# Performance work log

Measured on AMD Instinct MI355X. Metric: run time of the kernel, lower is better.

The kernel has to match this reference:

```python
import jax, jax.numpy as jnp
import numpy as np

N, E, X_DIM, EA_DIM, HID, NL, NC, NGRAPH = 50000, 800000, 64, 16, 64, 3, 10, 64
BN_EPS = 1e-5
STD_EPS = 1e-5


def setup_inputs() -> dict:
    key = jax.random.key(0)
    ks = jax.random.split(key, 24)
    w = lambda k, sh: (jax.random.normal(k, sh, jnp.float32) * 0.05)
    inp = {
        'x': jax.random.normal(ks[0], (N, X_DIM), jnp.float32),
        'edge_index': jax.random.randint(ks[1], (2, E), 0, N),
        'batch': jnp.sort(jax.random.randint(ks[2], (N,), 0, NGRAPH)),
        'edge_attr': jax.random.normal(ks[3], (E, EA_DIM), jnp.float32),
        # node / edge encoders
        'node_w': w(ks[4], (X_DIM, HID)), 'node_b': jnp.zeros((HID,), jnp.float32),
        'edge_w': w(ks[5], (EA_DIM, HID)), 'edge_b': jnp.zeros((HID,), jnp.float32),
        # per-layer PNA post_nn Linear(12*3*HID -> HID) and BatchNorm
        'conv_w': w(ks[6], (NL, 12 * 3 * HID, HID)), 'conv_b': jnp.zeros((NL, HID), jnp.float32),
        'bn_g': jnp.ones((NL, HID), jnp.float32), 'bn_b': jnp.zeros((NL, HID), jnp.float32),
        # fc_out: HID -> HID/2 -> HID/4 -> NC
        'fc1_w': w(ks[7], (HID, HID // 2)), 'fc1_b': jnp.zeros((HID // 2,), jnp.float32),
        'fc2_w': w(ks[8], (HID // 2, HID // 4)), 'fc2_b': jnp.zeros((HID // 4,), jnp.float32),
        'fc3_w': w(ks[9], (HID // 4, NC)), 'fc3_b': jnp.zeros((NC,), jnp.float32),
    }
    return inp


def _pna_layer(x, src, dst, ea, deg, degc, log_deg, avg_log, w, b):
    # message: concat([x_i, x_j, edge_attr]) with x_i = x[dst], x_j = x[src]  -> [E, 3H]
    h = jnp.concatenate([x[dst], x[src], ea], axis=-1)
    inv = (1.0 / degc)[:, None]
    s1 = jax.ops.segment_sum(h, dst, num_segments=N)
    mean = s1 * inv
    mean_sq = jax.ops.segment_sum(h * h, dst, num_segments=N) * inv
    std = jnp.sqrt(jax.nn.relu(mean_sq - mean * mean) + STD_EPS)
    has = (deg > 0)[:, None]
    mx = jax.ops.segment_max(h, dst, num_segments=N)
    mx = jnp.where(has, mx, 0.0)
    mn = -jax.ops.segment_max(-h, dst, num_segments=N)
    mn = jnp.where(has, mn, 0.0)
    out = jnp.concatenate([mean, mn, mx, std], axis=-1)  # [N, 4*3H]
    amp = (log_deg / avg_log)[:, None]
    att = (avg_log / log_deg)[:, None]
    out = jnp.concatenate([out, out * amp, out * att], axis=-1)  # [N, 12*3H]
    return out @ w + b


def reference(x, edge_index, batch, edge_attr, node_w, node_b, edge_w, edge_b,
              conv_w, conv_b, bn_g, bn_b, fc1_w, fc1_b, fc2_w, fc2_b, fc3_w, fc3_b):
    src, dst = edge_index[0], edge_index[1]
    x = x @ node_w + node_b
    ea = edge_attr @ edge_w + edge_b
    deg = jax.ops.segment_sum(jnp.ones((E,), jnp.float32), dst, num_segments=N)
    degc = jnp.maximum(deg, 1.0)
    log_deg = jnp.log(degc + 1.0)
    # avg of log(deg+1) over nodes (equivalent to the histogram-based avg_deg['log'])
    avg_log = jnp.mean(jnp.log(deg + 1.0))
    for i in range(NL):
        h = _pna_layer(x, src, dst, ea, deg, degc, log_deg, avg_log, conv_w[i], conv_b[i])
        mu = jnp.mean(h, axis=0)
        var = jnp.mean((h - mu) ** 2, axis=0)  # biased var, as torch BN training mode
        h = (h - mu) * jax.lax.rsqrt(var + BN_EPS) * bn_g[i] + bn_b[i]
        x = jax.nn.relu(h) + x  # dropout is identity in eval
    # global mean pool over graphs
    gsum = jax.ops.segment_sum(x, batch, num_segments=NGRAPH)
    gcnt = jnp.maximum(jax.ops.segment_sum(jnp.ones((N,), jnp.float32), batch, num_segments=NGRAPH), 1.0)
    g = gsum / gcnt[:, None]
    g = jax.nn.relu(g @ fc1_w + fc1_b)
    g = jax.nn.relu(g @ fc2_w + fc2_b)
    return g @ fc3_w + fc3_b
```

## Files before the change

kernel.cpp:

```cpp
#include <hip/hip_runtime.h>
#include <math.h>

#define N_NODES 50000
#define N_EDGES 800000
#define NGRAPH  64
#define KEFF    576

typedef short bf16x8 __attribute__((ext_vector_type(8)));
typedef float f32x4  __attribute__((ext_vector_type(4)));

__device__ inline unsigned short f2bf_rne(float f) {
  unsigned u = __float_as_uint(f);
  unsigned r = u + 0x7FFFu + ((u >> 16) & 1u);
  return (unsigned short)(r >> 16);
}
__device__ inline float bf2f(unsigned short h) {
  return __uint_as_float(((unsigned)h) << 16);
}


__global__ __launch_bounds__(256) void zero_kernel(
    int* __restrict__ cnt, float* __restrict__ gsum,
    double* __restrict__ bnacc, double* __restrict__ avgacc)
{
  int i = blockIdx.x * 256 + threadIdx.x;
  if (i < N_NODES) { cnt[i] = 0; return; }
  int j = i - N_NODES;
  if (j < NGRAPH * 64) { gsum[j] = 0.f; return; }
  int k = j - NGRAPH * 64;
  if (k < 3 * 128) { bnacc[k] = 0.0; return; }
  if (k == 3 * 128) *avgacc = 0.0;
}

__global__ __launch_bounds__(256) void node_enc_kernel(
    const float* __restrict__ xin, const float* __restrict__ nw,
    const float* __restrict__ nb, float* __restrict__ x)
{
  __shared__ float xs[256];
  int tid = threadIdx.x;
  int base = blockIdx.x * 256;
  xs[tid] = xin[base + tid];
  __syncthreads();
  int r = tid >> 6, j = tid & 63;
  float acc = nb[j];
#pragma unroll
  for (int t = 0; t < 64; t++) acc = fmaf(xs[r * 64 + t], nw[t * 64 + j], acc);
  x[base + tid] = acc;
}

__global__ void count_kernel(const int* __restrict__ dst, int* __restrict__ cnt)
{
  int e = blockIdx.x * 256 + threadIdx.x;
  atomicAdd(&cnt[dst[e]], 1);
}

__global__ __launch_bounds__(256) void scan_a_kernel(
    const int* __restrict__ cnt, int* __restrict__ bsum)
{
  __shared__ int s[256];
  int i = blockIdx.x * 256 + threadIdx.x;
  s[threadIdx.x] = (i < N_NODES) ? cnt[i] : 0;
  __syncthreads();
  for (int off = 128; off > 0; off >>= 1) {
    if (threadIdx.x < off) s[threadIdx.x] += s[threadIdx.x + off];
    __syncthreads();
  }
  if (threadIdx.x == 0) bsum[blockIdx.x] = s[0];
}

__global__ __launch_bounds__(256) void scan_b_kernel(
    const int* __restrict__ bsum, int* __restrict__ boff)
{
  __shared__ int s[256];
  int tid = threadIdx.x;
  int v = (tid < 196) ? bsum[tid] : 0;
  s[tid] = v;
  __syncthreads();
  for (int off = 1; off < 256; off <<= 1) {
    int t = (tid >= off) ? s[tid - off] : 0;
    __syncthreads();
    s[tid] += t;
    __syncthreads();
  }
  boff[tid] = s[tid] - v;
}

__global__ __launch_bounds__(256) void scan_c_kernel(
    const int* __restrict__ cnt, const int* __restrict__ boff,
    int* __restrict__ row_ptr, int* __restrict__ cursor)
{
  __shared__ int s[256];
  int tid = threadIdx.x;
  int i = blockIdx.x * 256 + tid;
  int v = (i < N_NODES) ? cnt[i] : 0;
  s[tid] = v;
  __syncthreads();
  for (int off = 1; off < 256; off <<= 1) {
    int t = (tid >= off) ? s[tid - off] : 0;
    __syncthreads();
    s[tid] += t;
    __syncthreads();
  }
  int incl = s[tid];
  int base = boff[blockIdx.x];
  if (i < N_NODES) { row_ptr[i] = base + incl - v; cursor[i] = base + incl - v; }
  if (i == N_NODES - 1) row_ptr[N_NODES] = base + incl;
}

__global__ void fill_kernel(const int* __restrict__ src, const int* __restrict__ dst,
                            int* __restrict__ cursor, int* __restrict__ srcs,
                            int* __restrict__ eids)
{
  int e = blockIdx.x * 256 + threadIdx.x;
  int d = dst[e];
  int pos = atomicAdd(&cursor[d], 1);
  srcs[pos] = src[e];
  eids[pos] = e;
}

__global__ __launch_bounds__(256) void deg_log_kernel(
    const int* __restrict__ cnt, float* __restrict__ log_deg,
    double* __restrict__ avgacc)
{
  __shared__ double sb[256];
  int i = blockIdx.x * 256 + threadIdx.x;
  double c = 0.0;
  if (i < N_NODES) {
    int d = cnt[i];
    int dc = d > 0 ? d : 1;
    log_deg[i] = logf((float)dc + 1.0f);
    c = (double)logf((float)d + 1.0f);
  }
  sb[threadIdx.x] = c;
  __syncthreads();
  for (int off = 128; off > 0; off >>= 1) {
    if (threadIdx.x < off) sb[threadIdx.x] += sb[threadIdx.x + off];
    __syncthreads();
  }
  if (threadIdx.x == 0) atomicAdd(avgacc, sb[0]);
}

__global__ void avg_gb_kernel(const double* __restrict__ avgacc,
                              float* __restrict__ avgf,
                              const int* __restrict__ batch,
                              int* __restrict__ gcnt)
{
  __shared__ int sb[65];
  int g = threadIdx.x;
  int lo = 0, hi = N_NODES;
  while (lo < hi) { int mid = (lo + hi) >> 1; if (batch[mid] < g) lo = mid + 1; else hi = mid; }
  sb[g] = lo;
  if (g == 0) { sb[64] = N_NODES; *avgf = (float)(*avgacc / (double)N_NODES); }
  __syncthreads();
  gcnt[g] = sb[g + 1] - sb[g];
}


__global__ __launch_bounds__(256) void wprep_kernel(
    const float* __restrict__ conv_w, unsigned short* __restrict__ wh,
    unsigned short* __restrict__ wl)
{
  int idx = blockIdx.x * 256 + threadIdx.x;
  int k = idx % 576;
  int c = (idx / 576) % 192;
  int l = idx / (576 * 192);
  int s = c >> 6, j = c & 63;
  const float* CW = conv_w + (size_t)l * 2304 * 64;
  float v;
  if (k < 64) {
    int base = s * 768 + k;
    v = CW[base * 64 + j] + CW[(base + 192) * 64 + j] + CW[(base + 384) * 64 + j];
  } else {
    const int srcseg[8] = {1, 2, 4, 5, 7, 8, 10, 11};
    int q = (k >> 6) - 1;
    int t = k & 63;
    v = CW[(s * 768 + srcseg[q] * 64 + t) * 64 + j];
  }
  unsigned short hh = f2bf_rne(v);
  size_t o = (((size_t)l * 12 + (c >> 4)) * 72 + (k >> 3)) * 128 + (c & 15) * 8 + (k & 7);
  wh[o] = hh;
  wl[o] = f2bf_rne(v - bf2f(hh));
}

__global__ void bprep_kernel(const float* __restrict__ conv_w, float* __restrict__ beff)
{
  int l = blockIdx.x;
  int s = threadIdx.x >> 6, j = threadIdx.x & 63;
  const float* CW = conv_w + (size_t)l * 2304 * 64 + (size_t)(s * 768 + 576) * 64;
  float sum = 0.f;
#pragma unroll
  for (int t = 0; t < 64; t++) sum += CW[t * 64 + j];
  beff[(l * 3 + s) * 64 + j] = sum * 0.0031622776601683794f;
}


__global__ __launch_bounds__(256) void agg_e_kernel(
    const float* __restrict__ eattr, const float* __restrict__ edge_w,
    const float* __restrict__ edge_b, const int* __restrict__ row_ptr,
    const int* __restrict__ eids,
    unsigned short* __restrict__ agg_h, unsigned short* __restrict__ agg_l)
{
  int lane = threadIdx.x & 63;
  int quad = lane >> 4, a16 = lane & 15;
  int n = blockIdx.x * 4 + (threadIdx.x >> 6);
  if (n >= N_NODES) return;
  float ew[16];
#pragma unroll
  for (int t = 0; t < 16; t++) ew[t] = edge_w[t * 64 + lane];
  float eb = edge_b[lane];
  int s0 = row_ptr[n], s1 = row_ptr[n + 1];
  float se = 0.f, qe = 0.f, mxe = -3.4e38f, mne = 3.4e38f;

  for (int j = s0; j < s1; j += 4) {
    int idx = j + quad;
    float av = 0.f;
    if (idx < s1) av = eattr[(size_t)eids[idx] * 16 + a16];
    unsigned au = __float_as_uint(av);
    float ea[4];
#pragma unroll
    for (int q = 0; q < 4; q++) {
      float c0 = eb, c1 = 0.f;
#pragma unroll
      for (int t = 0; t < 8; t++) {
        c0 = fmaf(__uint_as_float(__builtin_amdgcn_readlane(au, q * 16 + t)), ew[t], c0);
        c1 = fmaf(__uint_as_float(__builtin_amdgcn_readlane(au, q * 16 + 8 + t)), ew[8 + t], c1);
      }
      ea[q] = c0 + c1;
    }
    int rem = s1 - j;
#pragma unroll
    for (int q = 0; q < 4; q++) {
      if (q < rem) {
        se += ea[q]; qe = fmaf(ea[q], ea[q], qe);
        mxe = fmaxf(mxe, ea[q]); mne = fminf(mne, ea[q]);
      }
    }
  }

  int deg = s1 - s0;
  float inv = 1.0f / fmaxf((float)deg, 1.0f);
  bool has = deg > 0;
  float m_e = se * inv, ms_e = qe * inv;
  float sd_e = sqrtf(fmaxf(ms_e - m_e * m_e, 0.f) + 1e-5f);
  float mx_e = has ? mxe : 0.f, mn_e = has ? mne : 0.f;

  unsigned short* bh = agg_h + (size_t)n * KEFF;
  unsigned short* bl = agg_l + (size_t)n * KEFF;
#define W2(off, val) { float _v = (val); unsigned short _h = f2bf_rne(_v); \
                       bh[(off) + lane] = _h; bl[(off) + lane] = f2bf_rne(_v - bf2f(_h)); }
  W2(128, m_e); W2(256, mn_e); W2(384, mx_e); W2(512, sd_e);
#undef W2
}


__global__ __launch_bounds__(256) void agg_x_kernel(
    const float* __restrict__ x, const int* __restrict__ srcs,
    const int* __restrict__ row_ptr,
    unsigned short* __restrict__ agg_h, unsigned short* __restrict__ agg_l)
{
  int lane = threadIdx.x & 63;
  int n = blockIdx.x * 4 + (threadIdx.x >> 6);
  if (n >= N_NODES) return;
  float xd = x[(size_t)n * 64 + lane];
  int s0 = row_ptr[n], s1 = row_ptr[n + 1];
  float sA = 0.f, sB = 0.f, sC = 0.f, sD = 0.f;
  float qA = 0.f, qB = 0.f, qC = 0.f, qD = 0.f;
  float mx0 = -3.4e38f, mx1 = -3.4e38f, mn0 = 3.4e38f, mn1 = 3.4e38f;
  int j = s0;
  for (; j + 7 < s1; j += 8) {
    int e0 = srcs[j],     e1 = srcs[j + 1], e2 = srcs[j + 2], e3 = srcs[j + 3];
    int e4 = srcs[j + 4], e5 = srcs[j + 5], e6 = srcs[j + 6], e7 = srcs[j + 7];
    float x0 = x[(size_t)e0 * 64 + lane];
    float x1 = x[(size_t)e1 * 64 + lane];
    float x2 = x[(size_t)e2 * 64 + lane];
    float x3 = x[(size_t)e3 * 64 + lane];
    float x4 = x[(size_t)e4 * 64 + lane];
    float x5 = x[(size_t)e5 * 64 + lane];
    float x6 = x[(size_t)e6 * 64 + lane];
    float x7 = x[(size_t)e7 * 64 + lane];
    sA += x0; sB += x1; sC += x2; sD += x3;
    sA += x4; sB += x5; sC += x6; sD += x7;
    qA = fmaf(x0, x0, qA); qB = fmaf(x1, x1, qB);
    qC = fmaf(x2, x2, qC); qD = fmaf(x3, x3, qD);
    qA = fmaf(x4, x4, qA); qB = fmaf(x5, x5, qB);
    qC = fmaf(x6, x6, qC); qD = fmaf(x7, x7, qD);
    mx0 = fmaxf(mx0, fmaxf(fmaxf(x0, x1), fmaxf(x2, x3)));
    mx1 = fmaxf(mx1, fmaxf(fmaxf(x4, x5), fmaxf(x6, x7)));
    mn0 = fminf(mn0, fminf(fminf(x0, x1), fminf(x2, x3)));
    mn1 = fminf(mn1, fminf(fminf(x4, x5), fminf(x6, x7)));
  }
  if (j < s1) {
    int last = s1 - 1;
    int rem = s1 - j;
    int e0 = srcs[j];
    int e1 = srcs[j + 1 < s1 ? j + 1 : last];
    int e2 = srcs[j + 2 < s1 ? j + 2 : last];
    int e3 = srcs[j + 3 < s1 ? j + 3 : last];
    int e4 = srcs[j + 4 < s1 ? j + 4 : last];
    int e5 = srcs[j + 5 < s1 ? j + 5 : last];
    int e6 = srcs[j + 6 < s1 ? j + 6 : last];
    int e7 = srcs[j + 7 < s1 ? j + 7 : last];
    float x0 = x[(size_t)e0 * 64 + lane];
    float x1 = x[(size_t)e1 * 64 + lane];
    float x2 = x[(size_t)e2 * 64 + lane];
    float x3 = x[(size_t)e3 * 64 + lane];
    float x4 = x[(size_t)e4 * 64 + lane];
    float x5 = x[(size_t)e5 * 64 + lane];
    float x6 = x[(size_t)e6 * 64 + lane];
    float x7 = x[(size_t)e7 * 64 + lane];
    mx0 = fmaxf(mx0, fmaxf(fmaxf(x0, x1), fmaxf(x2, x3)));
    mx1 = fmaxf(mx1, fmaxf(fmaxf(x4, x5), fmaxf(x6, x7)));
    mn0 = fminf(mn0, fminf(fminf(x0, x1), fminf(x2, x3)));
    mn1 = fminf(mn1, fminf(fminf(x4, x5), fminf(x6, x7)));
    float z1 = 1 < rem ? x1 : 0.f;
    float z2 = 2 < rem ? x2 : 0.f;
    float z3 = 3 < rem ? x3 : 0.f;
    float z4 = 4 < rem ? x4 : 0.f;
    float z5 = 5 < rem ? x5 : 0.f;
    float z6 = 6 < rem ? x6 : 0.f;
    float z7 = 7 < rem ? x7 : 0.f;
    sA += x0; sB += z1; sC += z2; sD += z3;
    sA += z4; sB += z5; sC += z6; sD += z7;
    qA = fmaf(x0, x0, qA); qB = fmaf(z1, z1, qB);
    qC = fmaf(z2, z2, qC); qD = fmaf(z3, z3, qD);
    qA = fmaf(z4, z4, qA); qB = fmaf(z5, z5, qB);
    qC = fmaf(z6, z6, qC); qD = fmaf(z7, z7, qD);
  }
  float sx = (sA + sB) + (sC + sD);
  float qx = (qA + qB) + (qC + qD);
  float mxx = fmaxf(mx0, mx1), mnx = fminf(mn0, mn1);

  int deg = s1 - s0;
  float inv = 1.0f / fmaxf((float)deg, 1.0f);
  bool has = deg > 0;
  float m_s = sx * inv, ms_s = qx * inv;
  float sd_s = sqrtf(fmaxf(ms_s - m_s * m_s, 0.f) + 1e-5f);
  float mx_s = has ? mxx : 0.f, mn_s = has ? mnx : 0.f;

  unsigned short* bh = agg_h + (size_t)n * KEFF;
  unsigned short* bl = agg_l + (size_t)n * KEFF;
#define W2(off, val) { float _v = (val); unsigned short _h = f2bf_rne(_v); \
                       bh[(off) + lane] = _h; bl[(off) + lane] = f2bf_rne(_v - bf2f(_h)); }
  W2(0,   has ? xd : 0.f);
  W2(64,  m_s); W2(192, mn_s); W2(320, mx_s); W2(448, sd_s);
#undef W2
}


__global__ __launch_bounds__(256, 3) void gemm_kernel(
    const unsigned short* __restrict__ Ah, const unsigned short* __restrict__ Al,
    const unsigned short* __restrict__ Wh, const unsigned short* __restrict__ Wl,
    const float* __restrict__ beff, const float* __restrict__ bias,
    const float* __restrict__ log_deg, const float* __restrict__ avg_ptr,
    float* __restrict__ h, double* __restrict__ bnacc)
{
  __shared__ __align__(16) short AsH[64 * 40], AsL[64 * 40];
  int tid = threadIdx.x;
  int lane = tid & 63, w = tid >> 6;
  int quad = lane >> 4, l15 = lane & 15;
  int n0 = blockIdx.x * 64;

  int arow = tid >> 2, ac = tid & 3;
  int an = n0 + arow; if (an >= N_NODES) an = N_NODES - 1;
  const unsigned short* gah = Ah + (size_t)an * KEFF + ac * 8;
  const unsigned short* gal = Al + (size_t)an * KEFF + ac * 8;

  const unsigned short* pbh[3];
  const unsigned short* pbl[3];
#pragma unroll
  for (int s = 0; s < 3; s++) {
    size_t cb = (size_t)(s * 4 + w) * 72 * 128 + l15 * 8;
    pbh[s] = Wh + cb;
    pbl[s] = Wl + cb;
  }

  f32x4 acc[4][3] = {};
  float4 rh = *(const float4*)(gah);
  float4 rl = *(const float4*)(gal);

  for (int k0 = 0; k0 < KEFF; k0 += 32) {
    int koff = ((k0 >> 3) + quad) * 128;
    bf16x8 bhf[3], blf[3];
#pragma unroll
    for (int s = 0; s < 3; s++) {
      bhf[s] = *(const bf16x8*)(pbh[s] + koff);
      blf[s] = *(const bf16x8*)(pbl[s] + koff);
    }
    *(float4*)(AsH + arow * 40 + ac * 8) = rh;
    *(float4*)(AsL + arow * 40 + ac * 8) = rl;
    if (k0 + 32 < KEFF) {
      rh = *(const float4*)(gah + k0 + 32);
      rl = *(const float4*)(gal + k0 + 32);
    }
    __syncthreads();

#pragma unroll
    for (int i = 0; i < 4; i++) {
      int row = i * 16 + l15;
      bf16x8 ah = *(const bf16x8*)(AsH + row * 40 + quad * 8);
      bf16x8 al = *(const bf16x8*)(AsL + row * 40 + quad * 8);
#pragma unroll
      for (int s = 0; s < 3; s++) {
        acc[i][s] = __builtin_amdgcn_mfma_f32_16x16x32_bf16(ah, bhf[s], acc[i][s], 0, 0, 0);
        acc[i][s] = __builtin_amdgcn_mfma_f32_16x16x32_bf16(al, bhf[s], acc[i][s], 0, 0, 0);
        acc[i][s] = __builtin_amdgcn_mfma_f32_16x16x32_bf16(ah, blf[s], acc[i][s], 0, 0, 0);
      }
    }
    __syncthreads();
  }

  float avg = *avg_ptr;
  int col = w * 16 + l15;
  float be0 = beff[col], be1 = beff[64 + col], be2 = beff[128 + col];
  float bi = bias[col];
  float ss = 0.f, sq = 0.f;
#pragma unroll
  for (int i = 0; i < 4; i++) {
#pragma unroll
    for (int r = 0; r < 4; r++) {
      int n = n0 + i * 16 + quad * 4 + r;
      if (n < N_NODES) {
        float ld = log_deg[n];
        float amp = ld / avg, att = avg / ld;
        float v = (acc[i][0][r] + be0) + amp * (acc[i][1][r] + be1)
                + att * (acc[i][2][r] + be2) + bi;
        h[(size_t)n * 64 + col] = v;
        ss += v; sq = fmaf(v, v, sq);
      }
    }
  }
  ss += __shfl_xor(ss, 16, 64); ss += __shfl_xor(ss, 32, 64);
  sq += __shfl_xor(sq, 16, 64); sq += __shfl_xor(sq, 32, 64);
  if (quad == 0) {
    atomicAdd(&bnacc[col], (double)ss);
    atomicAdd(&bnacc[64 + col], (double)sq);
  }
}


__global__ __launch_bounds__(256) void apply_kernel(
    const float* __restrict__ h, const double* __restrict__ acc,
    const float* __restrict__ g, const float* __restrict__ bnb,
    float* __restrict__ x)
{
  __shared__ float smu[64], ssc[64];
  int tid = threadIdx.x;
  if (tid < 64) {
    double mu = acc[tid] / (double)N_NODES;
    double var = acc[64 + tid] / (double)N_NODES - mu * mu;
    double rstd = 1.0 / sqrt(var + 1e-5);
    smu[tid] = (float)mu;
    ssc[tid] = (float)(rstd * (double)g[tid]);
  }
  __syncthreads();
  int i4 = blockIdx.x * 256 + tid;
  const float4* h4 = (const float4*)h;
  float4* x4 = (float4*)x;
  int c4 = (i4 & 15) * 4;
  float4 hv = h4[i4], xv = x4[i4];
  float4 bb = ((const float4*)bnb)[i4 & 15];
  float4 r;
  r.x = fmaxf((hv.x - smu[c4])     * ssc[c4]     + bb.x, 0.f) + xv.x;
  r.y = fmaxf((hv.y - smu[c4 + 1]) * ssc[c4 + 1] + bb.y, 0.f) + xv.y;
  r.z = fmaxf((hv.z - smu[c4 + 2]) * ssc[c4 + 2] + bb.z, 0.f) + xv.z;
  r.w = fmaxf((hv.w - smu[c4 + 3]) * ssc[c4 + 3] + bb.w, 0.f) + xv.w;
  x4[i4] = r;
}


__global__ __launch_bounds__(256) void pool_kernel(
    const float* __restrict__ x, const int* __restrict__ batch,
    float* __restrict__ gsum)
{
  int tid = threadIdx.x;
  int j = tid & 63, ri = tid >> 6;
  float acc = 0.f; int cur = -1;
  for (int k = 0; k < 16; k++) {
    int n = blockIdx.x * 64 + k * 4 + ri;
    if (n < N_NODES) {
      int b = batch[n];
      if (b != cur) {
        if (cur >= 0) atomicAdd(&gsum[cur * 64 + j], acc);
        cur = b; acc = 0.f;
      }
      acc += x[(size_t)n * 64 + j];
    }
  }
  if (cur >= 0) atomicAdd(&gsum[cur * 64 + j], acc);
}

__global__ void fc_kernel(const float* __restrict__ gsum, const int* __restrict__ gcnt,
                          const float* __restrict__ w1, const float* __restrict__ b1,
                          const float* __restrict__ w2, const float* __restrict__ b2,
                          const float* __restrict__ w3, const float* __restrict__ b3,
                          float* __restrict__ out)
{
  int g = threadIdx.x;
  float cnt = fmaxf((float)gcnt[g], 1.0f);
  float gv[64];
#pragma unroll
  for (int j = 0; j < 64; j++) gv[j] = gsum[g * 64 + j] / cnt;
  float a1[32];
#pragma unroll
  for (int o = 0; o < 32; o++) {
    float s = b1[o];
#pragma unroll
    for (int j = 0; j < 64; j++) s = fmaf(gv[j], w1[j * 32 + o], s);
    a1[o] = fmaxf(s, 0.f);
  }
  float a2[16];
#pragma unroll
  for (int o = 0; o < 16; o++) {
    float s = b2[o];
#pragma unroll
    for (int j = 0; j < 32; j++) s = fmaf(a1[j], w2[j * 16 + o], s);
    a2[o] = fmaxf(s, 0.f);
  }
#pragma unroll
  for (int o = 0; o < 10; o++) {
    float s = b3[o];
#pragma unroll
    for (int j = 0; j < 16; j++) s = fmaf(a2[j], w3[j * 10 + o], s);
    out[g * 10 + o] = s;
  }
}


extern "C" void kernel_launch(void* const* d_in, const int* in_sizes, int n_in,
                              void* d_out, int out_size, void* d_ws, size_t ws_size,
                              hipStream_t stream)
{
  (void)in_sizes; (void)n_in; (void)out_size; (void)ws_size;
  const float* xin    = (const float*)d_in[0];
  const int*   ei     = (const int*)d_in[1];
  const int*   batch  = (const int*)d_in[2];
  const float* eattr  = (const float*)d_in[3];
  const float* node_w = (const float*)d_in[4];
  const float* node_b = (const float*)d_in[5];
  const float* edge_w = (const float*)d_in[6];
  const float* edge_b = (const float*)d_in[7];
  const float* conv_w = (const float*)d_in[8];
  const float* conv_b = (const float*)d_in[9];
  const float* bn_g   = (const float*)d_in[10];
  const float* bn_b   = (const float*)d_in[11];
  const float* fc1_w  = (const float*)d_in[12];
  const float* fc1_b  = (const float*)d_in[13];
  const float* fc2_w  = (const float*)d_in[14];
  const float* fc2_b  = (const float*)d_in[15];
  const float* fc3_w  = (const float*)d_in[16];
  const float* fc3_b  = (const float*)d_in[17];
  float* out = (float*)d_out;
  const int* srcp = ei;
  const int* dstp = ei + N_EDGES;

  char* p = (char*)d_ws;
  auto alloc = [&](size_t b) { char* r = p; p += (b + 255) & ~(size_t)255; return (void*)r; };
  float*  x       = (float*)alloc((size_t)N_NODES * 64 * 4);
  float*  h       = (float*)alloc((size_t)N_NODES * 64 * 4);
  unsigned short* agg_h = (unsigned short*)alloc((size_t)N_NODES * KEFF * 2);
  unsigned short* agg_l = (unsigned short*)alloc((size_t)N_NODES * KEFF * 2);
  unsigned short* wh    = (unsigned short*)alloc((size_t)3 * 12 * 72 * 128 * 2);
  unsigned short* wl    = (unsigned short*)alloc((size_t)3 * 12 * 72 * 128 * 2);
  int*    srcs    = (int*)alloc((size_t)N_EDGES * 4);
  int*    eids    = (int*)alloc((size_t)N_EDGES * 4);
  float*  beff    = (float*)alloc((size_t)3 * 3 * 64 * 4);
  int*    row_ptr = (int*)alloc((N_NODES + 1) * 4);
  int*    cursor  = (int*)alloc((size_t)N_NODES * 4);
  int*    cnt     = (int*)alloc((size_t)N_NODES * 4);
  float*  log_deg = (float*)alloc((size_t)N_NODES * 4);
  int*    bsum    = (int*)alloc(256 * 4);
  int*    boff    = (int*)alloc(256 * 4);
  double* avgacc  = (double*)alloc(256);
  float*  avgf    = (float*)alloc(256);
  double* bnacc   = (double*)alloc(3 * 128 * 8);
  float*  gsum    = (float*)alloc((size_t)NGRAPH * 64 * 4);
  int*    gcnt    = (int*)alloc((size_t)NGRAPH * 4);

  zero_kernel<<<213, 256, 0, stream>>>(cnt, gsum, bnacc, avgacc);
  node_enc_kernel<<<12500, 256, 0, stream>>>(xin, node_w, node_b, x);
  count_kernel<<<3125, 256, 0, stream>>>(dstp, cnt);
  scan_a_kernel<<<196, 256, 0, stream>>>(cnt, bsum);
  scan_b_kernel<<<1, 256, 0, stream>>>(bsum, boff);
  scan_c_kernel<<<196, 256, 0, stream>>>(cnt, boff, row_ptr, cursor);
  fill_kernel<<<3125, 256, 0, stream>>>(srcp, dstp, cursor, srcs, eids);
  deg_log_kernel<<<196, 256, 0, stream>>>(cnt, log_deg, avgacc);
  avg_gb_kernel<<<1, 64, 0, stream>>>(avgacc, avgf, batch, gcnt);
  wprep_kernel<<<1296, 256, 0, stream>>>(conv_w, wh, wl);
  bprep_kernel<<<3, 192, 0, stream>>>(conv_w, beff);

  agg_e_kernel<<<12500, 256, 0, stream>>>(eattr, edge_w, edge_b, row_ptr,
                                          eids, agg_h, agg_l);

  for (int l = 0; l < 3; l++) {
    agg_x_kernel<<<12500, 256, 0, stream>>>(x, srcs, row_ptr, agg_h, agg_l);
    gemm_kernel<<<782, 256, 0, stream>>>(agg_h, agg_l,
                                         wh + (size_t)l * 12 * 72 * 128,
                                         wl + (size_t)l * 12 * 72 * 128,
                                         beff + l * 192, conv_b + l * 64,
                                         log_deg, avgf, h, bnacc + l * 128);
    apply_kernel<<<3125, 256, 0, stream>>>(h, bnacc + l * 128, bn_g + l * 64,
                                           bn_b + l * 64, x);
  }

  pool_kernel<<<782, 256, 0, stream>>>(x, batch, gsum);
  fc_kernel<<<1, 64, 0, stream>>>(gsum, gcnt, fc1_w, fc1_b, fc2_w, fc2_b,
                                  fc3_w, fc3_b, out);
}
```

Before: 677.2 us.

## Compute per-edge encoder projection with split-bf16 MFMA in agg_e_kernel

Replaces the scalar readlane/FMA edge-attribute projection in the edge aggregation kernel with 16x16x32 bf16 MFMA instructions. Edge attributes and edge weights are split into high/low bf16 parts to approximate fp32 accuracy, and 16 edges are processed per MFMA tile, with partial statistics reduced across quads by shuffles. The bias is applied after aggregation, since the statistics shift by it and the std is unchanged. This cuts VALU work per edge but adds conversion overhead, a tail tile with masking, and some precision loss from the split-bf16 products.

```diff
diff --git a/kernel.cpp b/kernel.cpp
--- a/kernel.cpp
+++ b/kernel.cpp
@@ -8,6 +8,8 @@
 
 typedef short bf16x8 __attribute__((ext_vector_type(8)));
 typedef float f32x4  __attribute__((ext_vector_type(4)));
+typedef unsigned int u32;
+typedef unsigned int u32x4 __attribute__((ext_vector_type(4)));
 
 __device__ inline unsigned short f2bf_rne(float f) {
   unsigned u = __float_as_uint(f);
@@ -16,6 +18,25 @@
 }
 __device__ inline float bf2f(unsigned short h) {
   return __uint_as_float(((unsigned)h) << 16);
+}
+
+__device__ inline u32 cvtpk_bf16(float a, float b) {
+  u32 r;
+  asm("v_cvt_pk_bf16_f32 %0, %1, %2" : "=v"(r) : "v"(a), "v"(b));
+  return r;
+}
+
+__device__ inline void split2(float a, float b, u32& ph, u32& pl) {
+  ph = cvtpk_bf16(a, b);
+  float ha = __uint_as_float(ph << 16);
+  float hb = __uint_as_float(ph & 0xFFFF0000u);
+  pl = cvtpk_bf16(a - ha, b - hb);
+}
+
+__device__ inline bf16x8 pack_bf(u32 w0, u32 w1, u32 w2, u32 w3) {
+  u32x4 t;
+  t.x = w0; t.y = w1; t.z = w2; t.w = w3;
+  return __builtin_bit_cast(bf16x8, t);
 }
 
 
@@ -194,6 +215,22 @@
 }
 
 
+__device__ inline bf16x8 load_afrag(const float* __restrict__ eattr,
+                                    const int* __restrict__ eids,
+                                    int idx, int quad, bool wantlo)
+{
+  int eid = eids[idx];
+  const float4* rp = (const float4*)(eattr + (size_t)eid * 16 + (quad & 1) * 8);
+  float4 r0 = rp[0], r1 = rp[1];
+  u32 h0, l0, h1, l1, h2, l2, h3, l3;
+  split2(r0.x, r0.y, h0, l0);
+  split2(r0.z, r0.w, h1, l1);
+  split2(r1.x, r1.y, h2, l2);
+  split2(r1.z, r1.w, h3, l3);
+  return pack_bf(wantlo ? l0 : h0, wantlo ? l1 : h1,
+                 wantlo ? l2 : h2, wantlo ? l3 : h3);
+}
+
 __global__ __launch_bounds__(256) void agg_e_kernel(
     const float* __restrict__ eattr, const float* __restrict__ edge_w,
     const float* __restrict__ edge_b, const int* __restrict__ row_ptr,
@@ -201,48 +238,92 @@
     unsigned short* __restrict__ agg_h, unsigned short* __restrict__ agg_l)
 {
   int lane = threadIdx.x & 63;
-  int quad = lane >> 4, a16 = lane & 15;
+  int quad = lane >> 4, l15 = lane & 15;
   int n = blockIdx.x * 4 + (threadIdx.x >> 6);
   if (n >= N_NODES) return;
-  float ew[16];
-#pragma unroll
-  for (int t = 0; t < 16; t++) ew[t] = edge_w[t * 64 + lane];
-  float eb = edge_b[lane];
+
+  bf16x8 wbh[4], wbl[4];
+  {
+    int krow = (quad & 1) * 8;
+#pragma unroll
+    for (int cb = 0; cb < 4; cb++) {
+      u32 h[4], l[4];
+#pragma unroll
+      for (int p = 0; p < 4; p++) {
+        float va = edge_w[(krow + 2 * p) * 64 + cb * 16 + l15];
+        float vb = edge_w[(krow + 2 * p + 1) * 64 + cb * 16 + l15];
+        split2(va, vb, h[p], l[p]);
+      }
+      wbh[cb] = pack_bf(h[0], h[1], h[2], h[3]);
+      wbl[cb] = pack_bf(l[0], l[1], l[2], l[3]);
+    }
+  }
+
   int s0 = row_ptr[n], s1 = row_ptr[n + 1];
-  float se = 0.f, qe = 0.f, mxe = -3.4e38f, mne = 3.4e38f;
-
-  for (int j = s0; j < s1; j += 4) {
-    int idx = j + quad;
-    float av = 0.f;
-    if (idx < s1) av = eattr[(size_t)eids[idx] * 16 + a16];
-    unsigned au = __float_as_uint(av);
-    float ea[4];
-#pragma unroll
-    for (int q = 0; q < 4; q++) {
-      float c0 = eb, c1 = 0.f;
-#pragma unroll
-      for (int t = 0; t < 8; t++) {
-        c0 = fmaf(__uint_as_float(__builtin_amdgcn_readlane(au, q * 16 + t)), ew[t], c0);
-        c1 = fmaf(__uint_as_float(__builtin_amdgcn_readlane(au, q * 16 + 8 + t)), ew[8 + t], c1);
+  float se[4] = {0.f, 0.f, 0.f, 0.f}, sq[4] = {0.f, 0.f, 0.f, 0.f};
+  float mx[4], mn[4];
+#pragma unroll
+  for (int cb = 0; cb < 4; cb++) { mx[cb] = -3.4e38f; mn[cb] = 3.4e38f; }
+
+  const f32x4 zero = {};
+  bool wantlo = quad >= 2;
+  int j = s0;
+  for (; j + 16 <= s1; j += 16) {
+    bf16x8 af = load_afrag(eattr, eids, j + l15, quad, wantlo);
+#pragma unroll
+    for (int cb = 0; cb < 4; cb++) {
+      f32x4 acc = __builtin_amdgcn_mfma_f32_16x16x32_bf16(af, wbh[cb], zero, 0, 0, 0);
+      acc = __builtin_amdgcn_mfma_f32_16x16x32_bf16(af, wbl[cb], acc, 0, 0, 0);
+#pragma unroll
+      for (int r = 0; r < 4; r++) {
+        float v = acc[r];
+        se[cb] += v; sq[cb] = fmaf(v, v, sq[cb]);
+        mx[cb] = fmaxf(mx[cb], v); mn[cb] = fminf(mn[cb], v);
       }
-      ea[q] = c0 + c1;
-    }
+    }
+  }
+  if (j < s1) {
     int rem = s1 - j;
-#pragma unroll
-    for (int q = 0; q < 4; q++) {
-      if (q < rem) {
-        se += ea[q]; qe = fmaf(ea[q], ea[q], qe);
-        mxe = fmaxf(mxe, ea[q]); mne = fminf(mne, ea[q]);
+    int idx = j + l15; if (idx > s1 - 1) idx = s1 - 1;
+    bf16x8 af = load_afrag(eattr, eids, idx, quad, wantlo);
+#pragma unroll
+    for (int cb = 0; cb < 4; cb++) {
+      f32x4 acc = __builtin_amdgcn_mfma_f32_16x16x32_bf16(af, wbh[cb], zero, 0, 0, 0);
+      acc = __builtin_amdgcn_mfma_f32_16x16x32_bf16(af, wbl[cb], acc, 0, 0, 0);
+#pragma unroll
+      for (int r = 0; r < 4; r++) {
+        float v = acc[r];
+        bool valid = (quad * 4 + r) < rem;
+        float vm = valid ? v : 0.f;
+        se[cb] += vm; sq[cb] = fmaf(vm, vm, sq[cb]);
+        mx[cb] = fmaxf(mx[cb], v); mn[cb] = fminf(mn[cb], v);
       }
     }
   }
+
+#pragma unroll
+  for (int cb = 0; cb < 4; cb++) {
+    se[cb] += __shfl_xor(se[cb], 16, 64); se[cb] += __shfl_xor(se[cb], 32, 64);
+    sq[cb] += __shfl_xor(sq[cb], 16, 64); sq[cb] += __shfl_xor(sq[cb], 32, 64);
+    mx[cb] = fmaxf(mx[cb], __shfl_xor(mx[cb], 16, 64));
+    mx[cb] = fmaxf(mx[cb], __shfl_xor(mx[cb], 32, 64));
+    mn[cb] = fminf(mn[cb], __shfl_xor(mn[cb], 16, 64));
+    mn[cb] = fminf(mn[cb], __shfl_xor(mn[cb], 32, 64));
+  }
+  float SE = quad == 0 ? se[0] : quad == 1 ? se[1] : quad == 2 ? se[2] : se[3];
+  float SQ = quad == 0 ? sq[0] : quad == 1 ? sq[1] : quad == 2 ? sq[2] : sq[3];
+  float MX = quad == 0 ? mx[0] : quad == 1 ? mx[1] : quad == 2 ? mx[2] : mx[3];
+  float MN = quad == 0 ? mn[0] : quad == 1 ? mn[1] : quad == 2 ? mn[2] : mn[3];
 
   int deg = s1 - s0;
   float inv = 1.0f / fmaxf((float)deg, 1.0f);
   bool has = deg > 0;
-  float m_e = se * inv, ms_e = qe * inv;
-  float sd_e = sqrtf(fmaxf(ms_e - m_e * m_e, 0.f) + 1e-5f);
-  float mx_e = has ? mxe : 0.f, mn_e = has ? mne : 0.f;
+  float eb = edge_b[lane];
+  float m0 = SE * inv, ms0 = SQ * inv;
+  float sd_e = sqrtf(fmaxf(ms0 - m0 * m0, 0.f) + 1e-5f);
+  float m_e = has ? m0 + eb : 0.f;
+  float mx_e = has ? MX + eb : 0.f;
+  float mn_e = has ? MN + eb : 0.f;
 
   unsigned short* bh = agg_h + (size_t)n * KEFF;
   unsigned short* bl = agg_l + (size_t)n * KEFF;
```

Measured after the change: 646.8 us. 4.5% less time.
